# Kernel optimization log

Hardware: AMD Instinct MI355X
Metric: run time of the kernel (lower is better)

## Reference

```python
import jax, jax.numpy as jnp
import numpy as np
from jax import lax

EGO, MEM, NOBJ = 64, 128, 20
EPS = 1e-5

def gru_cell(x, h, w_ih, w_hh, b_ih, b_hh):
    # x: [..., EGO], h: [..., MEM]; torch GRUCell gate order r,z,n
    gi = jnp.einsum('...c,gc->...g', x, w_ih) + b_ih
    gh = jnp.einsum('...c,gc->...g', h, w_hh) + b_hh
    ir, iz, inn = jnp.split(gi, 3, axis=-1)
    hr, hz, hn = jnp.split(gh, 3, axis=-1)
    r = jax.nn.sigmoid(ir + hr)
    z = jax.nn.sigmoid(iz + hz)
    n = jnp.tanh(inn + r * hn)
    return (1.0 - z) * n + z * h

def conv(x, w, pad):
    return lax.conv_general_dilated(x, w, (1, 1), [(pad, pad), (pad, pad)],
                                    dimension_numbers=('NCHW', 'OIHW', 'NCHW'))

def bn(x, g, b):
    # training-mode BatchNorm2d: batch stats over (N,H,W)
    mu = jnp.mean(x, axis=(0, 2, 3), keepdims=True)
    var = jnp.var(x, axis=(0, 2, 3), keepdims=True)
    return (x - mu) * lax.rsqrt(var + EPS) * g[None, :, None, None] + b[None, :, None, None]

def setup_inputs() -> dict:
    key = jax.random.key(0)
    ks = jax.random.split(key, 16)
    noise = 0.01
    inp = {
        'features': jax.random.normal(ks[0], (2, 4, 256, 256, EGO), jnp.float32),
        'masks_inliers': jax.random.randint(ks[1], (2, 4, 256, 256), 0, 2, jnp.int32),
        'w_ih': jax.random.uniform(ks[2], (3 * MEM, EGO), jnp.float32, -noise, noise),
        'w_hh': jax.random.uniform(ks[3], (3 * MEM, MEM), jnp.float32, -noise, noise),
        'b_ih': jax.random.uniform(ks[4], (3 * MEM,), jnp.float32, -noise, noise),
        'b_hh': jnp.zeros((3 * MEM,), jnp.float32),
        'conv1_w': jax.random.normal(ks[5], (128, MEM, 7, 7), jnp.float32) * 0.02,
        'bn1_g': jnp.ones((128,), jnp.float32), 'bn1_b': jnp.zeros((128,), jnp.float32),
        'conv2_w': jax.random.normal(ks[6], (64, 128, 3, 3), jnp.float32) * 0.02,
        'bn2_g': jnp.ones((64,), jnp.float32), 'bn2_b': jnp.zeros((64,), jnp.float32),
        'conv3_w': jax.random.normal(ks[7], (48, 64, 3, 3), jnp.float32) * 0.02,
        'bn3_g': jnp.ones((48,), jnp.float32), 'bn3_b': jnp.zeros((48,), jnp.float32),
        'obj1_w': jax.random.normal(ks[8], (48, 48, 3, 3), jnp.float32) * 0.02,
        'bn4_g': jnp.ones((48,), jnp.float32), 'bn4_b': jnp.zeros((48,), jnp.float32),
        'obj2_w': jax.random.normal(ks[9], (NOBJ, 48, 1, 1), jnp.float32) * 0.02,
        'obj2_b': jnp.zeros((NOBJ,), jnp.float32),
    }
    return inp

def reference(features, masks_inliers, w_ih, w_hh, b_ih, b_hh,
              conv1_w, bn1_g, bn1_b, conv2_w, bn2_g, bn2_b,
              conv3_w, bn3_g, bn3_b, obj1_w, bn4_g, bn4_b, obj2_w, obj2_b):
    N = features.shape[0]
    state0 = jnp.zeros((N, 256, 256, MEM), jnp.float32)
    obs0 = jnp.zeros((N, 256, 256), jnp.int32)

    feats_t = jnp.moveaxis(features, 1, 0)       # [T,N,256,256,EGO]
    masks_t = jnp.moveaxis(masks_inliers, 1, 0)  # [T,N,256,256]

    def step(carry, xs):
        state, obs = carry
        feat, inl = xs
        m = inl > 0                               # [N,256,256]
        any_n = jnp.any(m, axis=(1, 2))           # [N]
        new_state = gru_cell(feat, state, w_ih, w_hh, b_ih, b_hh)
        state = jnp.where(m[..., None], new_state, state)
        obs = obs + inl * any_n[:, None, None].astype(inl.dtype)
        return (state, obs), None

    (state, observed_masks), _ = lax.scan(step, (state0, obs0), (feats_t, masks_t))

    memory = jnp.transpose(state, (0, 3, 1, 2))   # NCHW
    # decoder
    x = jax.nn.relu(bn(conv(memory, conv1_w, 3), bn1_g, bn1_b))
    x = jax.nn.relu(bn(conv(x, conv2_w, 1), bn2_g, bn2_b))
    x = jax.nn.relu(bn(conv(x, conv3_w, 1), bn3_g, bn3_b))
    x = jax.nn.relu(bn(conv(x, obj1_w, 1), bn4_g, bn4_b))
    semmap = conv(x, obj2_w, 0) + obj2_b[None, :, None, None]
    return semmap, observed_masks
```

## Files before the change

kernel.cpp:

```cpp
#include <hip/hip_runtime.h>
#include <hip/hip_bf16.h>
#include <math.h>

#define HWSZ 65536
#define NPIX 131072
#define LDA 208

typedef __attribute__((ext_vector_type(8))) short short8;
typedef __attribute__((ext_vector_type(4))) float f32x4;

__device__ __forceinline__ float sigmf(float x){ return 1.f/(1.f+__expf(-x)); }
__device__ __forceinline__ float tanhf2(float x){
  x = fminf(fmaxf(x,-15.f),15.f);
  float e = __expf(2.f*x);
  return (e-1.f)/(e+1.f);
}
__device__ __forceinline__ unsigned short f2b(float f){
  __hip_bfloat16 b = __float2bfloat16(f);
  return *(unsigned short*)&b;
}
__device__ __forceinline__ float b2f(unsigned short u){
  unsigned int v = ((unsigned int)u)<<16;
  return __uint_as_float(v);
}

__global__ void prep_gru_wb(const float* __restrict__ wih, const float* __restrict__ whh,
                            unsigned short* __restrict__ WG){
  int idx = blockIdx.x*256+threadIdx.x;
  if(idx >= 6*384*32) return;
  int kq = idx&31; int r = idx>>5;
  int c = r%384; int ch = r/384;
  int k = ch*32+kq;
  float v = (k<64) ? wih[c*64+k] : whh[c*128+(k-64)];
  WG[idx] = f2b(v);
}

__global__ void prep_conv_w(const float* __restrict__ src, unsigned short* __restrict__ dst,
                            int IC, int ICC, int OC, int KS, int total){
  int idx = blockIdx.x*256+threadIdx.x;
  if(idx>=total) return;
  int icq = idx&31; int r = idx>>5;
  int oc = r%OC; r/=OC;
  int ch = r%ICC; int tap = r/ICC;
  int ky = tap/KS, kx = tap%KS;
  int ic = ch*32+icq;
  float v = (ic<IC)? src[((oc*IC+ic)*KS+ky)*KS+kx] : 0.f;
  dst[idx] = f2b(v);
}

__global__ void flags_kernel(const int* __restrict__ masks, int* __restrict__ flags){
  __shared__ int red[256];
  int b = blockIdx.x; int acc=0;
  const int* m = masks + b*HWSZ;
  for(int i=threadIdx.x;i<HWSZ;i+=256) acc |= (m[i]>0)?1:0;
  red[threadIdx.x]=acc; __syncthreads();
  for(int s=128;s>0;s>>=1){ if(threadIdx.x<s) red[threadIdx.x]|=red[threadIdx.x+s]; __syncthreads(); }
  if(threadIdx.x==0) flags[b]=red[0];
}

__global__ void obs_kernel(const int* __restrict__ masks, const int* __restrict__ flags,
                           float* __restrict__ out){
  int p = blockIdx.x*256+threadIdx.x;
  if(p>=NPIX) return;
  int n = p>>16, hw = p&65535;
  int s=0;
  #pragma unroll
  for(int t=0;t<4;t++) s += masks[((n*4+t)<<16)+hw]*flags[n*4+t];
  out[p]=(float)s;
}

__launch_bounds__(512,4)
__global__ void gru_mfma(const float* __restrict__ feat, const int* __restrict__ masks,
                         const unsigned short* __restrict__ WG,
                         const float* __restrict__ bih, const float* __restrict__ bhh,
                         unsigned short* __restrict__ S){
  __shared__ __align__(16) unsigned short ax[32*LDA];
  __shared__ int msk[32];
  const int tid=threadIdx.x, wv=tid>>6, lane=tid&63, l15=lane&15, quad=lane>>4;
  const int p0=blockIdx.x*32;
  const int n=p0>>16, hw0=p0&65535;
  const int j16=wv*16;

  const int j=j16+l15;
  const float brv = bih[j]     + bhh[j];
  const float bzv = bih[128+j] + bhh[128+j];
  const float binv= bih[256+j];
  const float bhnv= bhh[256+j];

  float4 z4={0.f,0.f,0.f,0.f};
  { int px=tid>>4, c8=tid&15; *(float4*)&ax[px*LDA+64+c8*8]=z4; }

  for(int t=0;t<4;t++){
    __syncthreads();
    { int px=tid>>4, c4=tid&15;
      float4 v=*(const float4*)&feat[(size_t)(((n*4+t)<<16)|(hw0+px))*64 + c4*4];
      ushort4 u; u.x=f2b(v.x);u.y=f2b(v.y);u.z=f2b(v.z);u.w=f2b(v.w);
      *(ushort4*)&ax[px*LDA+c4*4]=u;
    }
    if(tid<32) msk[tid]=masks[((n*4+t)<<16)+hw0+tid];
    __syncthreads();

    f32x4 aR[2],aZ[2],aNX[2],aNH[2];
    #pragma unroll
    for(int mt=0;mt<2;mt++){
      f32x4 zz={0.f,0.f,0.f,0.f};
      aR[mt]=zz; aZ[mt]=zz; aNX[mt]=zz; aNH[mt]=zz;
    }

    #pragma unroll
    for(int ch=0;ch<6;ch++){
      short8 a[2];
      #pragma unroll
      for(int mt=0;mt<2;mt++)
        a[mt]=*(const short8*)&ax[(mt*16+l15)*LDA + ch*32 + quad*8];
      const unsigned short* bb = WG + (((size_t)(ch*384 + l15))<<5) + quad*8;
      short8 bR=*(const short8*)(bb + (((size_t)(     j16))<<5));
      short8 bZ=*(const short8*)(bb + (((size_t)(128+j16))<<5));
      short8 bN=*(const short8*)(bb + (((size_t)(256+j16))<<5));
      #pragma unroll
      for(int mt=0;mt<2;mt++){
        aR[mt]=__builtin_amdgcn_mfma_f32_16x16x32_bf16(a[mt],bR,aR[mt],0,0,0);
        aZ[mt]=__builtin_amdgcn_mfma_f32_16x16x32_bf16(a[mt],bZ,aZ[mt],0,0,0);
        if(ch<2)
          aNX[mt]=__builtin_amdgcn_mfma_f32_16x16x32_bf16(a[mt],bN,aNX[mt],0,0,0);
        else
          aNH[mt]=__builtin_amdgcn_mfma_f32_16x16x32_bf16(a[mt],bN,aNH[mt],0,0,0);
      }
    }
    __syncthreads();

    #pragma unroll
    for(int mt=0;mt<2;mt++){
      #pragma unroll
      for(int r=0;r<4;r++){
        int px=mt*16+quad*4+r;
        float rg=sigmf(aR[mt][r]+brv);
        float zg=sigmf(aZ[mt][r]+bzv);
        float nn=tanhf2(aNX[mt][r]+binv+rg*(aNH[mt][r]+bhnv));
        unsigned short hu=ax[px*LDA+64+j];
        float hold=b2f(hu);
        float h2=(1.f-zg)*nn+zg*hold;
        ax[px*LDA+64+j] = (msk[px]>0)? f2b(h2) : hu;
      }
    }
  }
  __syncthreads();
  { int px=tid>>4, c8=tid&15;
    *(float4*)&S[(size_t)(p0+px)*128 + c8*8] = *(float4*)&ax[px*LDA+64+c8*8];
  }
}

template<int IC,int ICP,int OC,int KS,int TPB,int WM,int WN>
__launch_bounds__(TPB, (TPB==512)?4:3)
__global__ void mconv(const unsigned short* __restrict__ in, const unsigned short* __restrict__ Wb,
                      unsigned short* __restrict__ out, float* __restrict__ partials){
  constexpr int P=KS/2, ROWS=128+KS-1, LDR=ICP+8, ICC=ICP/32, C8=ICP/8;
  constexpr int MT = 128/(WM*16);
  constexpr int OCW = OC/WN;
  constexpr int NTW = OCW/16;
  constexpr int NS = KS*ICC;
  constexpr int RPS = WM*4;
  __shared__ __align__(16) unsigned short lds[ROWS*LDR];
  const int tid=threadIdx.x;
  const int wv=tid>>6, lane=tid&63, l15=lane&15, quad=lane>>4;
  const int wm=wv/WN, wn=wv%WN;
  const int p0=blockIdx.x*128;
  const int n=p0>>16; const int hw0=p0&65535; const int y0=hw0>>8, x0=hw0&255;

  f32x4 acc[MT][NTW];
  #pragma unroll
  for(int mt=0;mt<MT;mt++)
    #pragma unroll
    for(int nn=0;nn<NTW;nn++){ f32x4 z={0.f,0.f,0.f,0.f}; acc[mt][nn]=z; }

  for(int ky=0;ky<KS;ky++){
    int ys=y0+ky-P;
    if(ys<0||ys>255) continue;
    __syncthreads();
    for(int i=tid;i<ROWS*C8;i+=TPB){
      int c8=i%C8, px=i/C8;
      int xg=x0-P+px;
      float4 v={0.f,0.f,0.f,0.f};
      if(xg>=0 && xg<256 && c8*8<IC)
        v = *(const float4*)(in + (size_t)(((n<<16)|(ys<<8))+xg)*IC + c8*8);
      *(float4*)&lds[px*LDR + c8*8] = v;
    }
    __syncthreads();

    short8 Bn[NTW];
    {
      const unsigned short* bp = Wb + ((size_t)(((ky*KS+0)*ICC+0)*OC + wn*OCW + l15)<<5) + quad*8;
      #pragma unroll
      for(int nn=0;nn<NTW;nn++) Bn[nn]=*(const short8*)(bp + (nn<<9));
    }
    #pragma unroll
    for(int s=0;s<NS;s++){
      const int kx=s/ICC, ch=s%ICC;
      short8 Bc[NTW];
      #pragma unroll
      for(int nn=0;nn<NTW;nn++) Bc[nn]=Bn[nn];
      if(s+1<NS){
        const int kx2=(s+1)/ICC, ch2=(s+1)%ICC;
        const unsigned short* bp = Wb + ((size_t)(((ky*KS+kx2)*ICC+ch2)*OC + wn*OCW + l15)<<5) + quad*8;
        #pragma unroll
        for(int nn=0;nn<NTW;nn++) Bn[nn]=*(const short8*)(bp + (nn<<9));
      }
      short8 a[MT];
      #pragma unroll
      for(int mt=0;mt<MT;mt++)
        a[mt]=*(const short8*)&lds[(wm*(MT*16) + mt*16 + l15 + kx)*LDR + ch*32 + quad*8];
      #pragma unroll
      for(int mt=0;mt<MT;mt++)
        #pragma unroll
        for(int nn=0;nn<NTW;nn++)
          acc[mt][nn]=__builtin_amdgcn_mfma_f32_16x16x32_bf16(a[mt],Bc[nn],acc[mt][nn],0,0,0);
    }
  }
  __syncthreads();

  #pragma unroll
  for(int mt=0;mt<MT;mt++){
    int pxb = p0 + wm*(MT*16) + mt*16 + quad*4;
    #pragma unroll
    for(int nn=0;nn<NTW;nn++){
      int oc = wn*OCW + nn*16 + l15;
      #pragma unroll
      for(int r=0;r<4;r++)
        out[(size_t)(pxb+r)*OC + oc] = f2b(acc[mt][nn][r]);
    }
  }

  float* ps=(float*)lds;
  int rps = wm*4+quad;
  #pragma unroll
  for(int nn=0;nn<NTW;nn++){
    float s1=0.f,s2=0.f;
    #pragma unroll
    for(int mt=0;mt<MT;mt++)
      #pragma unroll
      for(int r=0;r<4;r++){ float v=acc[mt][nn][r]; s1+=v; s2+=v*v; }
    ps[rps*OC + wn*OCW + nn*16+l15]=s1;
    ps[(RPS+rps)*OC + wn*OCW + nn*16+l15]=s2;
  }
  __syncthreads();
  if(tid<OC){
    float t1=0.f,t2=0.f;
    #pragma unroll
    for(int g=0;g<RPS;g++){ t1+=ps[g*OC+tid]; t2+=ps[(RPS+g)*OC+tid]; }
    partials[(size_t)blockIdx.x*2*OC+tid]=t1;
    partials[(size_t)blockIdx.x*2*OC+OC+tid]=t2;
  }
}

__global__ void stats_kernel(const float* __restrict__ partials, const float* __restrict__ g,
                             const float* __restrict__ b, float2* __restrict__ stats, int OC, int NB){
  __shared__ float r1[256], r2[256];
  int oc=blockIdx.x; int tid=threadIdx.x;
  float s1=0.f,s2=0.f;
  for(int bl=tid;bl<NB;bl+=256){ s1+=partials[(size_t)bl*2*OC+oc]; s2+=partials[(size_t)bl*2*OC+OC+oc]; }
  r1[tid]=s1;r2[tid]=s2; __syncthreads();
  for(int s=128;s>0;s>>=1){ if(tid<s){r1[tid]+=r1[tid+s]; r2[tid]+=r2[tid+s];} __syncthreads(); }
  if(tid==0){
    float mean=r1[0]*(1.f/131072.f);
    float var =r2[0]*(1.f/131072.f)-mean*mean;
    float sc=g[oc]*rsqrtf(var+1e-5f);
    float2 st; st.x=sc; st.y=b[oc]-mean*sc;
    stats[oc]=st;
  }
}

__global__ void bnrelu_b2b(const unsigned short* __restrict__ src, unsigned short* __restrict__ dst,
                           const float2* __restrict__ stats, int OC8, int total8){
  for(int i=blockIdx.x*256+threadIdx.x;i<total8;i+=gridDim.x*256){
    int c8=i%OC8;
    float4 v=((const float4*)src)[i];
    const unsigned short* us=(const unsigned short*)&v;
    float4 o;
    unsigned short* od=(unsigned short*)&o;
    #pragma unroll
    for(int j=0;j<8;j++){
      float2 s=stats[c8*8+j];
      od[j]=f2b(fmaxf(0.f, b2f(us[j])*s.x+s.y));
    }
    ((float4*)dst)[i]=o;
  }
}

__global__ void obj2_kernel(const unsigned short* __restrict__ in, const float* __restrict__ w,
                            const float* __restrict__ bias, float* __restrict__ out){
  __shared__ float wsm[20*48];
  __shared__ float bs[20];
  int tid=threadIdx.x;
  for(int i=tid;i<20*48;i+=256) wsm[i]=w[i];
  if(tid<20) bs[tid]=bias[tid];
  __syncthreads();
  int p=blockIdx.x*256+tid;
  int n=p>>16, hw=p&65535;
  float x[48];
  #pragma unroll
  for(int i=0;i<6;i++){
    float4 v=*(const float4*)&in[(size_t)p*48+i*8];
    const unsigned short* us=(const unsigned short*)&v;
    #pragma unroll
    for(int j=0;j<8;j++) x[i*8+j]=b2f(us[j]);
  }
  #pragma unroll
  for(int o=0;o<20;o++){
    float s=bs[o];
    #pragma unroll
    for(int c=0;c<48;c++) s+=x[c]*wsm[o*48+c];
    out[(size_t)((n*20+o)<<16)+hw]=s;
  }
}

extern "C" void kernel_launch(void* const* d_in, const int* in_sizes, int n_in,
                              void* d_out, int out_size, void* d_ws, size_t ws_size,
                              hipStream_t stream) {
  const float* feat = (const float*)d_in[0];
  const int*   masks= (const int*)  d_in[1];
  const float* w_ih = (const float*)d_in[2];
  const float* w_hh = (const float*)d_in[3];
  const float* b_ih = (const float*)d_in[4];
  const float* b_hh = (const float*)d_in[5];
  const float* c1w  = (const float*)d_in[6];
  const float* bn1g = (const float*)d_in[7];  const float* bn1b=(const float*)d_in[8];
  const float* c2w  = (const float*)d_in[9];
  const float* bn2g = (const float*)d_in[10]; const float* bn2b=(const float*)d_in[11];
  const float* c3w  = (const float*)d_in[12];
  const float* bn3g = (const float*)d_in[13]; const float* bn3b=(const float*)d_in[14];
  const float* o1w  = (const float*)d_in[15];
  const float* bn4g = (const float*)d_in[16]; const float* bn4b=(const float*)d_in[17];
  const float* o2w  = (const float*)d_in[18]; const float* o2b =(const float*)d_in[19];

  char* ws = (char*)d_ws;
  unsigned short* Rb  = (unsigned short*)(ws + 0);
  unsigned short* A1b = (unsigned short*)(ws + 33554432);
  unsigned short* A3b = A1b;
  unsigned short* Sb  = (unsigned short*)(ws + 67108864);
  unsigned short* A2b = Sb;
  unsigned short* A4b = Sb;
  unsigned short* W1b = (unsigned short*)(ws + 100663296);
  unsigned short* W2b = (unsigned short*)(ws + 102268928);
  unsigned short* W3b = (unsigned short*)(ws + 102416384);
  unsigned short* W4b = (unsigned short*)(ws + 102471680);
  unsigned short* WGb = (unsigned short*)(ws + 102526976);
  float* partials = (float*)(ws + 102674432);
  float2* stats   = (float2*)(ws + 103723008);
  int*   flags    = (int*)  (ws + 103724032);

  float* semmap = (float*)d_out;
  float* obsout = (float*)d_out + 2621440;

  prep_gru_wb<<<288,256,0,stream>>>(w_ih,w_hh,WGb);
  prep_conv_w<<<(49*4*128*32+255)/256,256,0,stream>>>(c1w,W1b,128,4,128,7,49*4*128*32);
  prep_conv_w<<<(9*4*64*32 +255)/256,256,0,stream>>>(c2w,W2b,128,4,64,3,9*4*64*32);
  prep_conv_w<<<(9*2*48*32 +255)/256,256,0,stream>>>(c3w,W3b,64,2,48,3,9*2*48*32);
  prep_conv_w<<<(9*2*48*32 +255)/256,256,0,stream>>>(o1w,W4b,48,2,48,3,9*2*48*32);

  flags_kernel<<<8,256,0,stream>>>(masks,flags);
  obs_kernel<<<512,256,0,stream>>>(masks,flags,obsout);

  gru_mfma<<<4096,512,0,stream>>>(feat,masks,WGb,b_ih,b_hh,Sb);

  mconv<128,128,128,7,512,2,4><<<1024,512,0,stream>>>(Sb,W1b,Rb,partials);
  stats_kernel<<<128,256,0,stream>>>(partials,bn1g,bn1b,stats,128,1024);
  bnrelu_b2b<<<4096,256,0,stream>>>(Rb,A1b,stats,16,NPIX*128/8);

  mconv<128,128,64,3,512,4,2><<<1024,512,0,stream>>>(A1b,W2b,Rb,partials);
  stats_kernel<<<64,256,0,stream>>>(partials,bn2g,bn2b,stats,64,1024);
  bnrelu_b2b<<<4096,256,0,stream>>>(Rb,A2b,stats,8,NPIX*64/8);

  mconv<64,64,48,3,256,4,1><<<1024,256,0,stream>>>(A2b,W3b,Rb,partials);
  stats_kernel<<<48,256,0,stream>>>(partials,bn3g,bn3b,stats,48,1024);
  bnrelu_b2b<<<4096,256,0,stream>>>(Rb,A3b,stats,6,NPIX*48/8);

  mconv<48,64,48,3,256,4,1><<<1024,256,0,stream>>>(A3b,W4b,Rb,partials);
  stats_kernel<<<48,256,0,stream>>>(partials,bn4g,bn4b,stats,48,1024);
  bnrelu_b2b<<<4096,256,0,stream>>>(Rb,A4b,stats,6,NPIX*48/8);

  obj2_kernel<<<512,256,0,stream>>>(A4b,o2w,o2b,semmap);
}
```

Measured before the change: 799.8 us.

## Use 32x32x16 bf16 MFMA conv kernel for conv1 and conv2

Adds a new implicit-GEMM conv kernel built on 32x32x16 bf16 MFMA tiles. Each of four waves owns 32 pixels, and weight fragments are software-prefetched one K-step ahead straight from global memory. Weights are repacked into 16-channel chunks to match this layout, and conv1 (7x7) and conv2 switch to it. The aim is fewer MFMA instructions per FLOP and less LDS traffic for B. In exchange, B now streams from global/L2 per wave and the accumulator register footprint grows, for example 4x16 floats for OC=128.

After: 810.9 us. No clear change (+1.4%).

```diff
diff --git a/kernel.cpp b/kernel.cpp
--- a/kernel.cpp
+++ b/kernel.cpp
@@ -8,6 +8,7 @@
 
 typedef __attribute__((ext_vector_type(8))) short short8;
 typedef __attribute__((ext_vector_type(4))) float f32x4;
+typedef __attribute__((ext_vector_type(16))) float f32x16;
 
 __device__ __forceinline__ float sigmf(float x){ return 1.f/(1.f+__expf(-x)); }
 __device__ __forceinline__ float tanhf2(float x){
@@ -48,6 +49,19 @@
   dst[idx] = f2b(v);
 }
 
+__global__ void prep_conv_w32(const float* __restrict__ src, unsigned short* __restrict__ dst,
+                              int IC, int OC, int KS, int total){
+  int idx = blockIdx.x*256+threadIdx.x;
+  if(idx>=total) return;
+  int q = idx&15; int r = idx>>4;
+  int oc = r%OC; r/=OC;
+  int ICC = IC/16;
+  int ch = r%ICC; int tap = r/ICC;
+  int ky = tap/KS, kx = tap%KS;
+  int ic = ch*16+q;
+  dst[idx] = f2b(src[((oc*IC+ic)*KS+ky)*KS+kx]);
+}
+
 __global__ void flags_kernel(const int* __restrict__ masks, int* __restrict__ flags){
   __shared__ int red[256];
   int b = blockIdx.x; int acc=0;
@@ -147,6 +161,96 @@
   __syncthreads();
   { int px=tid>>4, c8=tid&15;
     *(float4*)&S[(size_t)(p0+px)*128 + c8*8] = *(float4*)&ax[px*LDA+64+c8*8];
+  }
+}
+
+template<int IC,int OC,int KS>
+__launch_bounds__(256,3)
+__global__ void m32conv(const unsigned short* __restrict__ in, const unsigned short* __restrict__ Wb,
+                        unsigned short* __restrict__ out, float* __restrict__ partials){
+  constexpr int P=KS/2, ROWS=128+KS-1, LDR=IC+8, ICC=IC/16, C8=IC/8;
+  constexpr int NTW=OC/32, NS=KS*ICC;
+  __shared__ __align__(16) unsigned short lds[ROWS*LDR];
+  const int tid=threadIdx.x;
+  const int wv=tid>>6, lane=tid&63, l31=lane&31, hf=lane>>5;
+  const int p0=blockIdx.x*128;
+  const int n=p0>>16; const int hw0=p0&65535; const int y0=hw0>>8, x0=hw0&255;
+  const int m0=wv*32;
+
+  f32x16 acc[NTW];
+  #pragma unroll
+  for(int nn=0;nn<NTW;nn++){
+    #pragma unroll
+    for(int r=0;r<16;r++) acc[nn][r]=0.f;
+  }
+
+  for(int ky=0;ky<KS;ky++){
+    int ys=y0+ky-P;
+    if(ys<0||ys>255) continue;
+    __syncthreads();
+    for(int i=tid;i<ROWS*C8;i+=256){
+      int c8=i%C8, px=i/C8;
+      int xg=x0-P+px;
+      float4 v={0.f,0.f,0.f,0.f};
+      if(xg>=0 && xg<256)
+        v = *(const float4*)(in + (size_t)(((n<<16)|(ys<<8))+xg)*IC + c8*8);
+      *(float4*)&lds[px*LDR + c8*8] = v;
+    }
+    __syncthreads();
+
+    short8 Bn[NTW];
+    {
+      const unsigned short* bp = Wb + (((size_t)((ky*KS+0)*ICC+0)*OC + l31)<<4) + hf*8;
+      #pragma unroll
+      for(int nn=0;nn<NTW;nn++) Bn[nn]=*(const short8*)(bp + (nn<<9));
+    }
+    #pragma unroll
+    for(int s=0;s<NS;s++){
+      const int kx=s/ICC, ch=s%ICC;
+      short8 Bc[NTW];
+      #pragma unroll
+      for(int nn=0;nn<NTW;nn++) Bc[nn]=Bn[nn];
+      if(s+1<NS){
+        const int kx2=(s+1)/ICC, ch2=(s+1)%ICC;
+        const unsigned short* bp = Wb + (((size_t)((ky*KS+kx2)*ICC+ch2)*OC + l31)<<4) + hf*8;
+        #pragma unroll
+        for(int nn=0;nn<NTW;nn++) Bn[nn]=*(const short8*)(bp + (nn<<9));
+      }
+      short8 a = *(const short8*)&lds[(m0 + l31 + kx)*LDR + ch*16 + hf*8];
+      #pragma unroll
+      for(int nn=0;nn<NTW;nn++)
+        acc[nn]=__builtin_amdgcn_mfma_f32_32x32x16_bf16(a,Bc[nn],acc[nn],0,0,0);
+    }
+  }
+  __syncthreads();
+
+  #pragma unroll
+  for(int nn=0;nn<NTW;nn++){
+    int oc = nn*32 + l31;
+    #pragma unroll
+    for(int r=0;r<16;r++){
+      int m = (r&3) + 8*(r>>2) + 4*hf;
+      out[(size_t)(p0+m0+m)*OC + oc] = f2b(acc[nn][r]);
+    }
+  }
+
+  float* ps=(float*)lds;
+  int rps = wv*2+hf;
+  #pragma unroll
+  for(int nn=0;nn<NTW;nn++){
+    float s1=0.f,s2=0.f;
+    #pragma unroll
+    for(int r=0;r<16;r++){ float v=acc[nn][r]; s1+=v; s2+=v*v; }
+    ps[rps*OC + nn*32+l31]=s1;
+    ps[(8+rps)*OC + nn*32+l31]=s2;
+  }
+  __syncthreads();
+  if(tid<OC){
+    float t1=0.f,t2=0.f;
+    #pragma unroll
+    for(int g=0;g<8;g++){ t1+=ps[g*OC+tid]; t2+=ps[(8+g)*OC+tid]; }
+    partials[(size_t)blockIdx.x*2*OC+tid]=t1;
+    partials[(size_t)blockIdx.x*2*OC+OC+tid]=t2;
   }
 }
 
@@ -352,8 +456,8 @@
   float* obsout = (float*)d_out + 2621440;
 
   prep_gru_wb<<<288,256,0,stream>>>(w_ih,w_hh,WGb);
-  prep_conv_w<<<(49*4*128*32+255)/256,256,0,stream>>>(c1w,W1b,128,4,128,7,49*4*128*32);
-  prep_conv_w<<<(9*4*64*32 +255)/256,256,0,stream>>>(c2w,W2b,128,4,64,3,9*4*64*32);
+  prep_conv_w32<<<(49*8*128*16+255)/256,256,0,stream>>>(c1w,W1b,128,128,7,49*8*128*16);
+  prep_conv_w32<<<(9*8*64*16 +255)/256,256,0,stream>>>(c2w,W2b,128,64,3,9*8*64*16);
   prep_conv_w<<<(9*2*48*32 +255)/256,256,0,stream>>>(c3w,W3b,64,2,48,3,9*2*48*32);
   prep_conv_w<<<(9*2*48*32 +255)/256,256,0,stream>>>(o1w,W4b,48,2,48,3,9*2*48*32);
 
@@ -362,11 +466,11 @@
 
   gru_mfma<<<4096,512,0,stream>>>(feat,masks,WGb,b_ih,b_hh,Sb);
 
-  mconv<128,128,128,7,512,2,4><<<1024,512,0,stream>>>(Sb,W1b,Rb,partials);
+  m32conv<128,128,7><<<1024,256,0,stream>>>(Sb,W1b,Rb,partials);
   stats_kernel<<<128,256,0,stream>>>(partials,bn1g,bn1b,stats,128,1024);
   bnrelu_b2b<<<4096,256,0,stream>>>(Rb,A1b,stats,16,NPIX*128/8);
 
-  mconv<128,128,64,3,512,4,2><<<1024,512,0,stream>>>(A1b,W2b,Rb,partials);
+  m32conv<128,64,3><<<1024,256,0,stream>>>(A1b,W2b,Rb,partials);
   stats_kernel<<<64,256,0,stream>>>(partials,bn2g,bn2b,stats,64,1024);
   bnrelu_b2b<<<4096,256,0,stream>>>(Rb,A2b,stats,8,NPIX*64/8);
 
```
